# Performance work log

Hardware: AMD Instinct MI355X
Metric: run time of the kernel (lower is better)

## Reference

```python
import jax, jax.numpy as jnp
import numpy as np

IN_FEATURES = 4096
OUT_FEATURES = 4096
RANK = 16
ALPHA = 32.0
SCALING = ALPHA / RANK


def setup_inputs() -> dict:
    key = jax.random.key(0)
    k_x, k_a, k_b = jax.random.split(key, 3)
    x = jax.random.normal(k_x, (4, 2048, IN_FEATURES), dtype=jnp.float32)
    # kaiming-uniform(a=sqrt(5)) for A: bound = sqrt(6/((1+5)*fan_in)) = 1/sqrt(fan_in)
    bound = 1.0 / np.sqrt(IN_FEATURES)
    lora_A = jax.random.uniform(k_a, (RANK, IN_FEATURES), dtype=jnp.float32,
                                minval=-bound, maxval=bound)
    # B is zero-init in the module; use small random values so gradients are non-trivial
    lora_B = jax.random.normal(k_b, (OUT_FEATURES, RANK), dtype=jnp.float32) * 0.01
    return {"x": x, "lora_A": lora_A, "lora_B": lora_B}


def reference(x, lora_A, lora_B):
    # dropout=0 -> identity. F.linear(x, B@A) == x @ A^T @ B^T; keep low-rank order.
    h = jnp.einsum('bsd,rd->bsr', x, lora_A)      # [B,S,rank]
    out = jnp.einsum('bsr,or->bso', h, lora_B)    # [B,S,out_features]
    return out * SCALING
```

## Files before the change

### kernel.cpp

```cpp
#include <hip/hip_runtime.h>


#define IN_F  4096
#define OUT_F 4096
#define RANK  16
#define KSPLIT 32
#define KSLICE 128

typedef __attribute__((ext_vector_type(8))) short short8;
typedef __attribute__((ext_vector_type(4))) float f32x4;

static __device__ __forceinline__ short f2bf(float f) {
    union { float f; unsigned u; } v; v.f = f;
    unsigned r = v.u + 0x7fff + ((v.u >> 16) & 1);
    return (short)(r >> 16);
}
static __device__ __forceinline__ float bf2f(short h) {
    union { unsigned u; float f; } v; v.u = ((unsigned)(unsigned short)h) << 16;
    return v.f;
}

__global__ __launch_bounds__(256) void k_stage1(const float* __restrict__ x,
                                                const float* __restrict__ A,
                                                float* __restrict__ hp) {
    const int tid  = threadIdx.x;
    const int w    = __builtin_amdgcn_readfirstlane(tid >> 6);
    const int lane = tid & 63;
    const int g    = blockIdx.x * 4 + w;
    const int rg   = g >> 5;
    const int ks   = g & (KSPLIT - 1);
    const int row0 = rg * 64;
    const int k0   = ks * KSLICE;
    const int n    = lane & 15;
    const int q    = lane >> 4;

    short8 Ahi[4], Alo[4];
#pragma unroll
    for (int kt = 0; kt < 4; ++kt) {
        const float* ap = A + (size_t)n * IN_F + k0 + kt * 32 + q * 8;
        const float4 a0 = *(const float4*)ap;
        const float4 a1 = *(const float4*)(ap + 4);
        const float av[8] = {a0.x, a0.y, a0.z, a0.w, a1.x, a1.y, a1.z, a1.w};
#pragma unroll
        for (int j = 0; j < 8; ++j) {
            const short hi = f2bf(av[j]);
            Ahi[kt][j] = hi;
            Alo[kt][j] = f2bf(av[j] - bf2f(hi));
        }
    }

    f32x4 acc[4];
#pragma unroll
    for (int rt = 0; rt < 4; ++rt) acc[rt] = (f32x4){0.f, 0.f, 0.f, 0.f};

#pragma unroll
    for (int rt = 0; rt < 4; ++rt) {
        const float* xr = x + (size_t)(row0 + rt * 16 + n) * IN_F + k0 + q * 8;
        float4 v0[4], v1[4];
#pragma unroll
        for (int kt = 0; kt < 4; ++kt) {
            v0[kt] = *(const float4*)(xr + kt * 32);
            v1[kt] = *(const float4*)(xr + kt * 32 + 4);
        }
#pragma unroll
        for (int kt = 0; kt < 4; ++kt) {
            const float xv[8] = {v0[kt].x, v0[kt].y, v0[kt].z, v0[kt].w,
                                 v1[kt].x, v1[kt].y, v1[kt].z, v1[kt].w};
            short8 xhi, xlo;
#pragma unroll
            for (int j = 0; j < 8; ++j) {
                const short hi = f2bf(xv[j]);
                xhi[j] = hi;
                xlo[j] = f2bf(xv[j] - bf2f(hi));
            }
            acc[rt] = __builtin_amdgcn_mfma_f32_16x16x32_bf16(xhi, Ahi[kt], acc[rt], 0, 0, 0);
            acc[rt] = __builtin_amdgcn_mfma_f32_16x16x32_bf16(xlo, Ahi[kt], acc[rt], 0, 0, 0);
            acc[rt] = __builtin_amdgcn_mfma_f32_16x16x32_bf16(xhi, Alo[kt], acc[rt], 0, 0, 0);
        }
    }

#pragma unroll
    for (int rt = 0; rt < 4; ++rt) {
#pragma unroll
        for (int r = 0; r < 4; ++r) {
            const int row = row0 + rt * 16 + q * 4 + r;
            hp[((size_t)ks * 8192 + row) * RANK + n] = acc[rt][r];
        }
    }
}

__global__ __launch_bounds__(256) void k_stage2(const float* __restrict__ hp,
                                                const float* __restrict__ B,
                                                float* __restrict__ out) {
    __shared__ float hs[16 * RANK];
    const int tid  = threadIdx.x;
    const int b    = blockIdx.x;
    const int row0 = (b >> 2) * 16;
    const int col  = (b & 3) * 1024 + tid * 4;

    {
        const float* src = hp + (size_t)row0 * RANK + tid;
        float s = 0.0f;
#pragma unroll
        for (int ks = 0; ks < KSPLIT; ++ks)
            s += src[(size_t)ks * 8192 * RANK];
        hs[tid] = 2.0f * s;
    }

    float4 breg[16];
    const float4* B4 = (const float4*)(B + (size_t)col * RANK);
#pragma unroll
    for (int i = 0; i < 16; ++i) breg[i] = B4[i];
    const float* bf = (const float*)breg;
    __syncthreads();

    for (int r = 0; r < 16; ++r) {
        const float4 h0 = *(const float4*)(hs + r * RANK);
        const float4 h1 = *(const float4*)(hs + r * RANK + 4);
        const float4 h2 = *(const float4*)(hs + r * RANK + 8);
        const float4 h3 = *(const float4*)(hs + r * RANK + 12);
        const float hv[16] = {h0.x, h0.y, h0.z, h0.w, h1.x, h1.y, h1.z, h1.w,
                              h2.x, h2.y, h2.z, h2.w, h3.x, h3.y, h3.z, h3.w};
        float4 acc = {0.f, 0.f, 0.f, 0.f};
#pragma unroll
        for (int rho = 0; rho < RANK; ++rho) {
            acc.x += hv[rho] * bf[0 * RANK + rho];
            acc.y += hv[rho] * bf[1 * RANK + rho];
            acc.z += hv[rho] * bf[2 * RANK + rho];
            acc.w += hv[rho] * bf[3 * RANK + rho];
        }
        *(float4*)(out + (size_t)(row0 + r) * OUT_F + col) = acc;
    }
}

extern "C" void kernel_launch(void* const* d_in, const int* in_sizes, int n_in,
                              void* d_out, int out_size, void* d_ws, size_t ws_size,
                              hipStream_t stream) {
    const float* x  = (const float*)d_in[0];
    const float* A  = (const float*)d_in[1];
    const float* Bm = (const float*)d_in[2];
    float* out = (float*)d_out;
    float* hp  = (float*)d_ws;

    k_stage1<<<1024, 256, 0, stream>>>(x, A, hp);
    k_stage2<<<2048, 256, 0, stream>>>(hp, Bm, out);
}
```

Measured before the change: 256.6 us.

## Fuse low-rank down and up projections into a single kernel

Replaces the two-kernel split-K pipeline with one kernel. Each 512-thread block owns 16 rows: eight waves each reduce a 512-wide K slice with split-bf16 MFMAs, the partials are summed in shared memory, and the block then multiplies by B and writes the output. This drops the global workspace round trip for the rank-16 partials and the second launch. In exchange, A is reloaded and reconverted in every block, each block handles fewer rows, and only 512 blocks run, which may limit latency hiding.

```diff
diff --git a/kernel.cpp b/kernel.cpp
--- a/kernel.cpp
+++ b/kernel.cpp
@@ -4,8 +4,6 @@
 #define IN_F  4096
 #define OUT_F 4096
 #define RANK  16
-#define KSPLIT 32
-#define KSLICE 128
 
 typedef __attribute__((ext_vector_type(8))) short short8;
 typedef __attribute__((ext_vector_type(4))) float f32x4;
@@ -20,116 +18,99 @@
     return v.f;
 }
 
-__global__ __launch_bounds__(256) void k_stage1(const float* __restrict__ x,
-                                                const float* __restrict__ A,
-                                                float* __restrict__ hp) {
+__global__ __launch_bounds__(512, 4) void k_fused(const float* __restrict__ x,
+                                                  const float* __restrict__ A,
+                                                  const float* __restrict__ B,
+                                                  float* __restrict__ out) {
+    __shared__ float hpart[8][16][16];
+    __shared__ float hs[16 * RANK];
+
     const int tid  = threadIdx.x;
     const int w    = __builtin_amdgcn_readfirstlane(tid >> 6);
     const int lane = tid & 63;
-    const int g    = blockIdx.x * 4 + w;
-    const int rg   = g >> 5;
-    const int ks   = g & (KSPLIT - 1);
-    const int row0 = rg * 64;
-    const int k0   = ks * KSLICE;
     const int n    = lane & 15;
     const int q    = lane >> 4;
+    const int row0 = blockIdx.x * 16;
+    const int k0   = w * 512;
 
-    short8 Ahi[4], Alo[4];
-#pragma unroll
-    for (int kt = 0; kt < 4; ++kt) {
-        const float* ap = A + (size_t)n * IN_F + k0 + kt * 32 + q * 8;
-        const float4 a0 = *(const float4*)ap;
-        const float4 a1 = *(const float4*)(ap + 4);
-        const float av[8] = {a0.x, a0.y, a0.z, a0.w, a1.x, a1.y, a1.z, a1.w};
-#pragma unroll
-        for (int j = 0; j < 8; ++j) {
-            const short hi = f2bf(av[j]);
-            Ahi[kt][j] = hi;
-            Alo[kt][j] = f2bf(av[j] - bf2f(hi));
-        }
-    }
+    f32x4 acc = {0.f, 0.f, 0.f, 0.f};
+    const float* xr = x + (size_t)(row0 + n) * IN_F + k0 + q * 8;
+    const float* ar = A + (size_t)n * IN_F + k0 + q * 8;
 
-    f32x4 acc[4];
-#pragma unroll
-    for (int rt = 0; rt < 4; ++rt) acc[rt] = (f32x4){0.f, 0.f, 0.f, 0.f};
-
-#pragma unroll
-    for (int rt = 0; rt < 4; ++rt) {
-        const float* xr = x + (size_t)(row0 + rt * 16 + n) * IN_F + k0 + q * 8;
-        float4 v0[4], v1[4];
+    for (int g = 0; g < 4; ++g) {
+        float4 a0[4], a1[4], v0[4], v1[4];
 #pragma unroll
         for (int kt = 0; kt < 4; ++kt) {
-            v0[kt] = *(const float4*)(xr + kt * 32);
-            v1[kt] = *(const float4*)(xr + kt * 32 + 4);
+            const float* ap = ar + (size_t)(g * 4 + kt) * 32;
+            const float* xp = xr + (size_t)(g * 4 + kt) * 32;
+            a0[kt] = *(const float4*)ap;
+            a1[kt] = *(const float4*)(ap + 4);
+            v0[kt] = *(const float4*)xp;
+            v1[kt] = *(const float4*)(xp + 4);
         }
 #pragma unroll
         for (int kt = 0; kt < 4; ++kt) {
+            const float av[8] = {a0[kt].x, a0[kt].y, a0[kt].z, a0[kt].w,
+                                 a1[kt].x, a1[kt].y, a1[kt].z, a1[kt].w};
             const float xv[8] = {v0[kt].x, v0[kt].y, v0[kt].z, v0[kt].w,
                                  v1[kt].x, v1[kt].y, v1[kt].z, v1[kt].w};
-            short8 xhi, xlo;
+            short8 Ahi, Alo, xhi, xlo;
 #pragma unroll
             for (int j = 0; j < 8; ++j) {
-                const short hi = f2bf(xv[j]);
-                xhi[j] = hi;
-                xlo[j] = f2bf(xv[j] - bf2f(hi));
+                const short ah = f2bf(av[j]);
+                Ahi[j] = ah;
+                Alo[j] = f2bf(av[j] - bf2f(ah));
+                const short xh = f2bf(xv[j]);
+                xhi[j] = xh;
+                xlo[j] = f2bf(xv[j] - bf2f(xh));
             }
-            acc[rt] = __builtin_amdgcn_mfma_f32_16x16x32_bf16(xhi, Ahi[kt], acc[rt], 0, 0, 0);
-            acc[rt] = __builtin_amdgcn_mfma_f32_16x16x32_bf16(xlo, Ahi[kt], acc[rt], 0, 0, 0);
-            acc[rt] = __builtin_amdgcn_mfma_f32_16x16x32_bf16(xhi, Alo[kt], acc[rt], 0, 0, 0);
+            acc = __builtin_amdgcn_mfma_f32_16x16x32_bf16(xhi, Ahi, acc, 0, 0, 0);
+            acc = __builtin_amdgcn_mfma_f32_16x16x32_bf16(xlo, Ahi, acc, 0, 0, 0);
+            acc = __builtin_amdgcn_mfma_f32_16x16x32_bf16(xhi, Alo, acc, 0, 0, 0);
         }
     }
 
 #pragma unroll
-    for (int rt = 0; rt < 4; ++rt) {
+    for (int r = 0; r < 4; ++r)
+        hpart[w][q * 4 + r][n] = acc[r];
+    __syncthreads();
+
+    if (tid < 256) {
+        const float* hp = &hpart[0][0][0];
+        float s = 0.f;
 #pragma unroll
-        for (int r = 0; r < 4; ++r) {
-            const int row = row0 + rt * 16 + q * 4 + r;
-            hp[((size_t)ks * 8192 + row) * RANK + n] = acc[rt][r];
-        }
-    }
-}
-
-__global__ __launch_bounds__(256) void k_stage2(const float* __restrict__ hp,
-                                                const float* __restrict__ B,
-                                                float* __restrict__ out) {
-    __shared__ float hs[16 * RANK];
-    const int tid  = threadIdx.x;
-    const int b    = blockIdx.x;
-    const int row0 = (b >> 2) * 16;
-    const int col  = (b & 3) * 1024 + tid * 4;
-
-    {
-        const float* src = hp + (size_t)row0 * RANK + tid;
-        float s = 0.0f;
-#pragma unroll
-        for (int ks = 0; ks < KSPLIT; ++ks)
-            s += src[(size_t)ks * 8192 * RANK];
+        for (int ww = 0; ww < 8; ++ww)
+            s += hp[ww * 256 + tid];
         hs[tid] = 2.0f * s;
     }
-
-    float4 breg[16];
-    const float4* B4 = (const float4*)(B + (size_t)col * RANK);
-#pragma unroll
-    for (int i = 0; i < 16; ++i) breg[i] = B4[i];
-    const float* bf = (const float*)breg;
     __syncthreads();
 
-    for (int r = 0; r < 16; ++r) {
-        const float4 h0 = *(const float4*)(hs + r * RANK);
-        const float4 h1 = *(const float4*)(hs + r * RANK + 4);
-        const float4 h2 = *(const float4*)(hs + r * RANK + 8);
-        const float4 h3 = *(const float4*)(hs + r * RANK + 12);
-        const float hv[16] = {h0.x, h0.y, h0.z, h0.w, h1.x, h1.y, h1.z, h1.w,
-                              h2.x, h2.y, h2.z, h2.w, h3.x, h3.y, h3.z, h3.w};
-        float4 acc = {0.f, 0.f, 0.f, 0.f};
 #pragma unroll
-        for (int rho = 0; rho < RANK; ++rho) {
-            acc.x += hv[rho] * bf[0 * RANK + rho];
-            acc.y += hv[rho] * bf[1 * RANK + rho];
-            acc.z += hv[rho] * bf[2 * RANK + rho];
-            acc.w += hv[rho] * bf[3 * RANK + rho];
+    for (int half = 0; half < 2; ++half) {
+        const int col = half * 2048 + tid * 4;
+        float4 breg[16];
+        const float4* B4 = (const float4*)(B + (size_t)col * RANK);
+#pragma unroll
+        for (int i = 0; i < 16; ++i) breg[i] = B4[i];
+        const float* bf = (const float*)breg;
+
+        for (int r = 0; r < 16; ++r) {
+            const float4 h0 = *(const float4*)(hs + r * RANK);
+            const float4 h1 = *(const float4*)(hs + r * RANK + 4);
+            const float4 h2 = *(const float4*)(hs + r * RANK + 8);
+            const float4 h3 = *(const float4*)(hs + r * RANK + 12);
+            const float hv[16] = {h0.x, h0.y, h0.z, h0.w, h1.x, h1.y, h1.z, h1.w,
+                                  h2.x, h2.y, h2.z, h2.w, h3.x, h3.y, h3.z, h3.w};
+            float4 o = {0.f, 0.f, 0.f, 0.f};
+#pragma unroll
+            for (int rho = 0; rho < RANK; ++rho) {
+                o.x += hv[rho] * bf[0 * RANK + rho];
+                o.y += hv[rho] * bf[1 * RANK + rho];
+                o.z += hv[rho] * bf[2 * RANK + rho];
+                o.w += hv[rho] * bf[3 * RANK + rho];
+            }
+            *(float4*)(out + (size_t)(row0 + r) * OUT_F + col) = o;
         }
-        *(float4*)(out + (size_t)(row0 + r) * OUT_F + col) = acc;
     }
 }
 
@@ -140,8 +121,6 @@
     const float* A  = (const float*)d_in[1];
     const float* Bm = (const float*)d_in[2];
     float* out = (float*)d_out;
-    float* hp  = (float*)d_ws;
 
-    k_stage1<<<1024, 256, 0, stream>>>(x, A, hp);
-    k_stage2<<<2048, 256, 0, stream>>>(hp, Bm, out);
+    k_fused<<<512, 512, 0, stream>>>(x, A, Bm, out);
 }
```

Measured after the change: 483.8 us. 88.6% more time.
